# Optimization experiments

Measured on AMD Instinct MI355X. Metric: run time of the kernel, lower is better.

## Reference

```python
import jax, jax.numpy as jnp
import numpy as np

B, T, R = 32, 200, 8192
TOPK_RATIO = 0.05
K = int(R * TOPK_RATIO)            # 409 selected regions
K2 = int(R * TOPK_RATIO ** 2)      # 20 compressed features
REST = R - K                        # 7783 == rest_limitation
BN_EPS = 1e-5
NORM_EPS = 1e-12


def _linear_params(key, fan_in, fan_out):
    kw, kb = jax.random.split(key)
    bound = 1.0 / np.sqrt(fan_in)
    w = jax.random.uniform(kw, (fan_out, fan_in), jnp.float32, -bound, bound)
    b = jax.random.uniform(kb, (fan_out,), jnp.float32, -bound, bound)
    return w, b


def setup_inputs() -> dict:
    key = jax.random.key(0)
    ks = jax.random.split(key, 8)
    x = jax.random.normal(ks[0], (B, T, R), jnp.float32)
    w_proj, b_proj = _linear_params(ks[1], T, 1)
    w_process, b_process = _linear_params(ks[2], K, K)
    w_compress, b_compress = _linear_params(ks[3], K, K2)
    w_unzip, b_unzip = _linear_params(ks[4], K2, K)
    w_unprocess, b_unprocess = _linear_params(ks[5], K, K)
    w_rest, b_rest = _linear_params(ks[6], K, REST)
    bn_gamma = jnp.ones((T,), jnp.float32)
    bn_beta = jnp.zeros((T,), jnp.float32)
    return {
        "x": x,
        "w_proj": w_proj[0], "b_proj": b_proj,
        "w_process": w_process, "b_process": b_process,
        "bn_gamma": bn_gamma, "bn_beta": bn_beta,
        "w_compress": w_compress, "b_compress": b_compress,
        "w_unzip": w_unzip, "b_unzip": b_unzip,
        "w_unprocess": w_unprocess, "b_unprocess": b_unprocess,
        "w_rest": w_rest, "b_rest": b_rest,
    }


def reference(x, w_proj, b_proj, w_process, b_process, bn_gamma, bn_beta,
              w_compress, b_compress, w_unzip, b_unzip,
              w_unprocess, b_unprocess, w_rest, b_rest):
    # ---------------- Encoder ----------------
    border_mask = jnp.isnan(x)                       # [B,T,R]
    x = jnp.where(border_mask, 0.0, x)
    # F.normalize over the time axis (dim=1)
    nrm = jnp.sqrt(jnp.sum(x * x, axis=1, keepdims=True))
    x = x / jnp.maximum(nrm, NORM_EPS)
    # projection: Linear(T,1) on x.transpose(-1,-2) -> score [B,R]
    score = jnp.einsum('btr,t->br', x, w_proj) + b_proj
    border_limit = jnp.mean(border_mask.astype(x.dtype), axis=1)   # [B,R]
    score = jnp.where(border_limit.astype(bool), -10000.0, score)
    _, index = jax.lax.top_k(score, K)               # [B,K] (descending score order)
    x_topk = jnp.take_along_axis(x, index[:, None, :], axis=2)  # [B,T,K]
    sel = jnp.zeros((B, R), x.dtype).at[jnp.arange(B)[:, None], index].set(1.0)
    mask = jnp.broadcast_to(sel[:, None, :], (B, T, R))
    # process: Linear(K,K) + BatchNorm1d(T) in training mode (batch stats)
    h = jnp.einsum('btk,jk->btj', x_topk, w_process) + b_process
    mu = jnp.mean(h, axis=(0, 2), keepdims=True)
    var = jnp.var(h, axis=(0, 2), keepdims=True)     # biased, as torch BN
    h = (h - mu) / jnp.sqrt(var + BN_EPS)
    h = h * bn_gamma[None, :, None] + bn_beta[None, :, None]
    x_compress = jnp.einsum('btk,jk->btj', h, w_compress) + b_compress  # [B,T,K2]

    # ---------------- Decoder ----------------
    z = jnp.einsum('btc,kc->btk', x_compress, w_unzip) + b_unzip
    z = jnp.einsum('btk,jk->btj', z, w_unprocess) + b_unprocess          # [B,T,K]
    z_rest = jnp.einsum('btk,rk->btr', z, w_rest) + b_rest               # [B,T,REST]
    # rest positions: columns neither NaN-bordered nor topk-selected, ascending
    occupied = jnp.logical_or(sel.astype(bool), jnp.any(border_mask, axis=1))  # [B,R]
    rest_pos = jax.vmap(lambda s: jnp.argsort(s)[:REST])(occupied)       # [B,REST]

    def scat(zv, zr, idx, rp):
        xr = jnp.zeros((T, R), zv.dtype)
        xr = xr.at[:, idx].set(zv)
        xr = xr.at[:, rp].set(zr)
        return xr

    x_recon = jax.vmap(scat)(z, z_rest, index, rest_pos)                 # [B,T,R]
    return (x_recon, x_compress, mask, border_mask, index)
```

## Files before the change

### kernel.cpp

```cpp
#include <hip/hip_runtime.h>

#define Bz 32
#define Tz 200
#define Rz 8192
#define Kz 409
#define KP 416
#define K2 20
#define K2P 32
#define RESTz 7783

typedef __bf16 bf16x8 __attribute__((ext_vector_type(8)));
typedef float f32x4 __attribute__((ext_vector_type(4)));

__launch_bounds__(256)
__global__ void k_padcast(const float* __restrict__ src, __bf16* __restrict__ dst,
                          int N, int Kd, int Npad, int Kpad) {
    int i = blockIdx.x * 256 + threadIdx.x;
    int total = Npad * Kpad;
    if (i >= total) return;
    int r = i / Kpad, c = i - r * Kpad;
    float v = (r < N && c < Kd) ? src[(size_t)r * Kd + c] : 0.f;
    dst[i] = (__bf16)v;
}

__launch_bounds__(256)
__global__ void k_wu(const float* __restrict__ wup, const float* __restrict__ wz,
                     const float* __restrict__ b_uz, const float* __restrict__ b_up,
                     float* __restrict__ WU_f, float* __restrict__ bU,
                     __bf16* __restrict__ WU_b) {
    __shared__ float lw[Kz * K2];
    __shared__ float lb[Kz];
    const int tid = threadIdx.x;
    for (int i = tid; i < Kz * K2; i += 256) lw[i] = wz[i];
    for (int i = tid; i < Kz; i += 256) lb[i] = b_uz[i];
    __syncthreads();
    const int r = blockIdx.x * 8 + (tid >> 5);
    const int c = tid & 31;
    if (r >= 512) return;
    if (r >= Kz) {
        WU_b[(size_t)r * K2P + c] = (__bf16)0.f;
        if (c == K2) bU[r] = 0.f;
        return;
    }
    const float* row = wup + (size_t)r * Kz;
    if (c < K2) {
        float a0 = 0.f, a1 = 0.f, a2 = 0.f, a3 = 0.f;
#pragma unroll 4
        for (int j = 0; j < 408; j += 4) {
            a0 = fmaf(row[j],     lw[(j)     * K2 + c], a0);
            a1 = fmaf(row[j + 1], lw[(j + 1) * K2 + c], a1);
            a2 = fmaf(row[j + 2], lw[(j + 2) * K2 + c], a2);
            a3 = fmaf(row[j + 3], lw[(j + 3) * K2 + c], a3);
        }
        a0 = fmaf(row[408], lw[408 * K2 + c], a0);
        float acc = (a0 + a1) + (a2 + a3);
        WU_f[(size_t)r * K2 + c] = acc;
        WU_b[(size_t)r * K2P + c] = (__bf16)acc;
    } else {
        WU_b[(size_t)r * K2P + c] = (__bf16)0.f;
        if (c == K2) {
            float a0 = 0.f, a1 = 0.f, a2 = 0.f, a3 = 0.f;
#pragma unroll 4
            for (int j = 0; j < 408; j += 4) {
                a0 = fmaf(row[j], lb[j], a0);
                a1 = fmaf(row[j + 1], lb[j + 1], a1);
                a2 = fmaf(row[j + 2], lb[j + 2], a2);
                a3 = fmaf(row[j + 3], lb[j + 3], a3);
            }
            a0 = fmaf(row[408], lb[408], a0);
            bU[r] = (a0 + a1) + (a2 + a3) + b_up[r];
        }
    }
}

__launch_bounds__(256)
__global__ void k_wr(const float* __restrict__ wr, const float* __restrict__ b_r,
                     const float* __restrict__ WU_f, const float* __restrict__ bU,
                     __bf16* __restrict__ WR_b, float* __restrict__ bR) {
    __shared__ float lw[Kz * K2];
    __shared__ float lb[Kz];
    const int tid = threadIdx.x;
    for (int i = tid; i < Kz * K2; i += 256) lw[i] = WU_f[i];
    for (int i = tid; i < Kz; i += 256) lb[i] = bU[i];
    __syncthreads();
    const int r = blockIdx.x * 8 + (tid >> 5);
    const int c = tid & 31;
    if (r >= 7808) return;
    if (r >= RESTz) {
        WR_b[(size_t)r * K2P + c] = (__bf16)0.f;
        if (c == K2) bR[r] = 0.f;
        return;
    }
    const float* row = wr + (size_t)r * Kz;
    if (c < K2) {
        float a0 = 0.f, a1 = 0.f, a2 = 0.f, a3 = 0.f;
#pragma unroll 4
        for (int j = 0; j < 408; j += 4) {
            a0 = fmaf(row[j],     lw[(j)     * K2 + c], a0);
            a1 = fmaf(row[j + 1], lw[(j + 1) * K2 + c], a1);
            a2 = fmaf(row[j + 2], lw[(j + 2) * K2 + c], a2);
            a3 = fmaf(row[j + 3], lw[(j + 3) * K2 + c], a3);
        }
        a0 = fmaf(row[408], lw[408 * K2 + c], a0);
        WR_b[(size_t)r * K2P + c] = (__bf16)((a0 + a1) + (a2 + a3));
    } else {
        WR_b[(size_t)r * K2P + c] = (__bf16)0.f;
        if (c == K2) {
            float a0 = 0.f, a1 = 0.f, a2 = 0.f, a3 = 0.f;
#pragma unroll 4
            for (int j = 0; j < 408; j += 4) {
                a0 = fmaf(row[j], lb[j], a0);
                a1 = fmaf(row[j + 1], lb[j + 1], a1);
                a2 = fmaf(row[j + 2], lb[j + 2], a2);
                a3 = fmaf(row[j + 3], lb[j + 3], a3);
            }
            a0 = fmaf(row[408], lb[408], a0);
            bR[r] = (a0 + a1) + (a2 + a3) + b_r[r];
        }
    }
}

__launch_bounds__(256)
__global__ void k_stats(const float* __restrict__ x, const float* __restrict__ w_proj,
                        const float* __restrict__ b_proj,
                        float* __restrict__ invnrm, float* __restrict__ score,
                        int* __restrict__ bordany, float* __restrict__ border_out) {
    const int b = blockIdx.y;
    const int c = blockIdx.x * 256 + threadIdx.x;
    const float* xp = x + (size_t)b * Tz * Rz + c;
    float* bp = border_out + (size_t)b * Tz * Rz + c;
    float p[32];
#pragma unroll
    for (int y = 0; y < 32; ++y) p[y] = 0.f;
    int nn = 0;
    for (int k = 0; k < 7; ++k) {
        const int tbase = k * 32;
#pragma unroll
        for (int y = 0; y < 32; ++y) {
            const int t = tbase + y;
            if (t < Tz) {
                float v = xp[(size_t)t * Rz];
                bool isn = (v != v);
                nn |= isn ? 1 : 0;
                float val = isn ? 0.f : v;
                bp[(size_t)t * Rz] = isn ? 1.0f : 0.0f;
                p[y] = __fadd_rn(p[y], __fmul_rn(val, val));
            }
        }
    }
#pragma unroll
    for (int off = 16; off > 0; off >>= 1)
#pragma unroll
        for (int y = 0; y < 16; ++y)
            if (y < off) p[y] = __fadd_rn(p[y], p[y + off]);
    const float ss = p[0];
    const float nv = fmaxf(__fsqrt_rn(ss), 1e-12f);
    float q[32];
#pragma unroll
    for (int y = 0; y < 32; ++y) q[y] = 0.f;
    for (int k = 0; k < 7; ++k) {
        const int tbase = k * 32;
#pragma unroll
        for (int y = 0; y < 32; ++y) {
            const int t = tbase + y;
            if (t < Tz) {
                float v = xp[(size_t)t * Rz];
                float val = (v != v) ? 0.f : v;
                float xn = __fdiv_rn(val, nv);
                float e = __fmul_rn(xn, w_proj[t]);
                q[y] = __fadd_rn(q[y], e);
            }
        }
    }
#pragma unroll
    for (int off = 16; off > 0; off >>= 1)
#pragma unroll
        for (int y = 0; y < 16; ++y)
            if (y < off) q[y] = __fadd_rn(q[y], q[y + off]);
    float sc = __fadd_rn(q[0], b_proj[0]);
    if (nn) sc = -10000.f;
    invnrm[(size_t)b * Rz + c] = __fdiv_rn(1.0f, nv);
    score[(size_t)b * Rz + c] = sc;
    bordany[(size_t)b * Rz + c] = nn;
}

__launch_bounds__(1024)
__global__ void k_topk(const float* __restrict__ score, const int* __restrict__ bordany,
                       int* __restrict__ index_ws, int* __restrict__ rest_pos,
                       float* __restrict__ o_index) {
    const int b = blockIdx.x;
    const int tid = threadIdx.x;
    __shared__ unsigned su[Rz];
    __shared__ unsigned hist[256];
    __shared__ unsigned sfx[256];
    __shared__ unsigned ckey[512];
    __shared__ unsigned cidx[512];
    __shared__ unsigned cnum;
    __shared__ unsigned sh_prefix;
    __shared__ int sh_need;
    __shared__ int scnt[1024];

    for (int i = tid; i < Rz; i += 1024) {
        unsigned u = __float_as_uint(score[(size_t)b * Rz + i]);
        u = (u & 0x80000000u) ? ~u : (u | 0x80000000u);
        su[i] = u;
    }
    __syncthreads();

    unsigned prefix = 0u, pmask = 0u;
    int need = Kz;
    for (int byte = 3; byte >= 0; --byte) {
        const int sh = byte * 8;
        if (tid < 256) hist[tid] = 0u;
        __syncthreads();
        for (int i = tid; i < Rz; i += 1024) {
            unsigned u = su[i];
            if ((u & pmask) == prefix) atomicAdd(&hist[(u >> sh) & 255u], 1u);
        }
        __syncthreads();
        if (tid < 256) sfx[tid] = hist[tid];
        __syncthreads();
        for (int off = 1; off < 256; off <<= 1) {
            unsigned add = 0u;
            if (tid < 256 && tid + off < 256) add = sfx[tid + off];
            __syncthreads();
            if (tid < 256) sfx[tid] += add;
            __syncthreads();
        }
        if (tid < 256) {
            unsigned above = (tid == 255) ? 0u : sfx[tid + 1];
            if (sfx[tid] >= (unsigned)need && above < (unsigned)need) {
                sh_need = need - (int)above;
                sh_prefix = prefix | ((unsigned)tid << sh);
            }
        }
        __syncthreads();
        prefix = sh_prefix;
        need = sh_need;
        pmask |= (0xFFu << sh);
        __syncthreads();
    }
    const unsigned Tval = prefix;

    if (tid == 0) cnum = 0u;
    __syncthreads();
    for (int i = tid; i < Rz; i += 1024) {
        unsigned u = su[i];
        if (u >= Tval) {
            unsigned p = atomicAdd(&cnum, 1u);
            if (p < 512u) { ckey[p] = u; cidx[p] = (unsigned)i; }
        }
    }
    __syncthreads();
    const int cn = (cnum < 512u) ? (int)cnum : 512;
    for (int i = tid; i < 512; i += 1024)
        if (i >= cn) { ckey[i] = 0u; cidx[i] = 0xFFFFFFFFu; }
    __syncthreads();

    for (int kk = 2; kk <= 512; kk <<= 1) {
        for (int j = kk >> 1; j > 0; j >>= 1) {
            if (tid < 256) {
                const int i = ((tid & ~(j - 1)) << 1) | (tid & (j - 1));
                const int l = i | j;
                unsigned ka = ckey[i], kb = ckey[l];
                unsigned ia = cidx[i], ib = cidx[l];
                bool a_after_b = (ka < kb) || (ka == kb && ia > ib);
                bool b_after_a = (kb < ka) || (kb == ka && ib > ia);
                bool desc = ((i & kk) == 0);
                bool dosw = desc ? a_after_b : b_after_a;
                if (dosw) { ckey[i] = kb; ckey[l] = ka; cidx[i] = ib; cidx[l] = ia; }
            }
            __syncthreads();
        }
    }

    for (int i = tid; i < Kz; i += 1024) {
        int idx = (int)(cidx[i] & 8191u);
        index_ws[b * Kz + i] = idx;
        o_index[(size_t)b * Kz + i] = (float)idx;
    }
    __syncthreads();
    for (int i = tid; i < Rz; i += 1024)
        su[i] = (bordany[(size_t)b * Rz + i] != 0) ? 1u : 0u;
    __syncthreads();
    for (int i = tid; i < Kz; i += 1024) su[cidx[i] & 8191u] = 1u;
    __syncthreads();
    int cnt = 0;
    {
        const int base = tid * 8;
#pragma unroll
        for (int o = 0; o < 8; ++o) cnt += (su[base + o] == 0u) ? 1 : 0;
    }
    scnt[tid] = cnt;
    __syncthreads();
    for (int offp = 1; offp < 1024; offp <<= 1) {
        int add = (tid >= offp) ? scnt[tid - offp] : 0;
        __syncthreads();
        scnt[tid] += add;
        __syncthreads();
    }
    const int total_un = scnt[1023];
    int run = scnt[tid] - cnt;
    const int base = tid * 8;
    for (int o = 0; o < 8; ++o) {
        const int c = base + o;
        const bool un = (su[c] == 0u);
        int pos = un ? run : (total_un + (c - run));
        if (un) run++;
        if (pos < RESTz) rest_pos[b * RESTz + pos] = c;
    }
}

__launch_bounds__(256)
__global__ void k_gather(const float* __restrict__ x, const float* __restrict__ invnrm,
                         const int* __restrict__ index_ws, __bf16* __restrict__ x_topk) {
    const int m = blockIdx.x;
    const int b = m / Tz;
    const float* xrow = x + (size_t)m * Rz;
    for (int kk = threadIdx.x; kk < KP; kk += 256) {
        float val = 0.f;
        if (kk < Kz) {
            const unsigned idx = (unsigned)index_ws[b * Kz + kk] & 8191u;
            float v = xrow[idx];
            if (v != v) v = 0.f;
            val = __fmul_rn(v, invnrm[(size_t)b * Rz + idx]);
        }
        x_topk[(size_t)m * KP + kk] = (__bf16)val;
    }
}

__launch_bounds__(256)
__global__ void k_bn(const __bf16* __restrict__ h, const float* __restrict__ gamma,
                     const float* __restrict__ beta, __bf16* __restrict__ hbn) {
    const int t = blockIdx.x;
    const int tid = threadIdx.x;
    float s = 0.f, s2 = 0.f;
    for (int i = tid; i < Bz * Kz; i += 256) {
        int b = i / Kz, j = i - b * Kz;
        float v = (float)h[(size_t)(b * Tz + t) * KP + j];
        s += v;
        s2 += v * v;
    }
    for (int off = 32; off > 0; off >>= 1) {
        s += __shfl_down(s, off);
        s2 += __shfl_down(s2, off);
    }
    __shared__ float rs[4], rs2[4];
    __shared__ float sc_sh, sf_sh;
    const int wid = tid >> 6;
    if ((tid & 63) == 0) { rs[wid] = s; rs2[wid] = s2; }
    __syncthreads();
    if (tid == 0) {
        float S = rs[0] + rs[1] + rs[2] + rs[3];
        float S2 = rs2[0] + rs2[1] + rs2[2] + rs2[3];
        const float invN = 1.f / (float)(Bz * Kz);
        float mu = S * invN;
        float var = S2 * invN - mu * mu;
        float rstd = rsqrtf(var + 1e-5f);
        float scl = gamma[t] * rstd;
        sc_sh = scl;
        sf_sh = beta[t] - mu * scl;
    }
    __syncthreads();
    const float scl = sc_sh, sft = sf_sh;
    for (int i = tid; i < Bz * KP; i += 256) {
        int b = i / KP, j = i - b * KP;
        float outv = 0.f;
        if (j < Kz) {
            float v = (float)h[(size_t)(b * Tz + t) * KP + j];
            outv = v * scl + sft;
        }
        hbn[(size_t)(b * Tz + t) * KP + j] = (__bf16)outv;
    }
}

__launch_bounds__(256)
__global__ void k_mask(const int* __restrict__ index_ws, float* __restrict__ o_mask) {
    const int bt = blockIdx.x;
    const int b = bt / Tz;
    const int tid = threadIdx.x;
    __shared__ unsigned bm[256];
    bm[tid] = 0u;
    __syncthreads();
    for (int i = tid; i < Kz; i += 256) {
        unsigned idx = (unsigned)index_ws[b * Kz + i] & 8191u;
        atomicOr(&bm[idx >> 5], 1u << (idx & 31u));
    }
    __syncthreads();
    const unsigned bits = bm[tid];
    float* dst = o_mask + (size_t)bt * Rz + tid * 32;
#pragma unroll
    for (int g = 0; g < 8; ++g) {
        float4 v;
        v.x = ((bits >> (g * 4 + 0)) & 1u) ? 1.0f : 0.0f;
        v.y = ((bits >> (g * 4 + 1)) & 1u) ? 1.0f : 0.0f;
        v.z = ((bits >> (g * 4 + 2)) & 1u) ? 1.0f : 0.0f;
        v.w = ((bits >> (g * 4 + 3)) & 1u) ? 1.0f : 0.0f;
        *(float4*)(dst + g * 4) = v;
    }
}

template <int EPI>
__launch_bounds__(256)
__global__ void k_gemm(const __bf16* __restrict__ A, int lda, int ksteps,
                       const __bf16* __restrict__ Wb, int ldb,
                       const float* __restrict__ bias,
                       __bf16* __restrict__ b_out,
                       float* __restrict__ o_xc,
                       const int* __restrict__ index_ws,
                       const int* __restrict__ rest_pos,
                       float* __restrict__ o_recon) {
    __shared__ __bf16 As[128][32];
    __shared__ __bf16 Bs[128][32];
    const int m0 = blockIdx.x * 128;
    const int n0 = blockIdx.y * 128;
    const int tid = threadIdx.x;
    const int lane = tid & 63;
    const int wid = tid >> 6;
    const int wm = wid >> 1, wn = wid & 1;
    const int r0 = lane >> 2;
    const int sg = (lane & 3) * 8;
    const int fr = lane & 15;
    const int fg = lane >> 4;
    f32x4 acc[4][4];
#pragma unroll
    for (int i = 0; i < 4; ++i)
#pragma unroll
        for (int j = 0; j < 4; ++j) {
            f32x4 z = {0.f, 0.f, 0.f, 0.f};
            acc[i][j] = z;
        }

    const int ca = wid * 16 + r0;
    const int cb = (wid + 4) * 16 + r0;
    const __bf16* gA0 = A + (size_t)(m0 + ca) * lda + sg;
    const __bf16* gA1 = A + (size_t)(m0 + cb) * lda + sg;
    const __bf16* gB0 = Wb + (size_t)(n0 + ca) * ldb + sg;
    const __bf16* gB1 = Wb + (size_t)(n0 + cb) * ldb + sg;
    __bf16* lA0 = &As[wid * 16][0];
    __bf16* lA1 = &As[(wid + 4) * 16][0];
    __bf16* lB0 = &Bs[wid * 16][0];
    __bf16* lB1 = &Bs[(wid + 4) * 16][0];

    for (int s = 0; s < ksteps; ++s) {
        const int k0 = s * 32;
        __syncthreads();
        __builtin_amdgcn_global_load_lds(gA0 + k0, lA0, 16, 0, 0);
        __builtin_amdgcn_global_load_lds(gA1 + k0, lA1, 16, 0, 0);
        __builtin_amdgcn_global_load_lds(gB0 + k0, lB0, 16, 0, 0);
        __builtin_amdgcn_global_load_lds(gB1 + k0, lB1, 16, 0, 0);
        __syncthreads();
        bf16x8 af[4], bf[4];
#pragma unroll
        for (int mi = 0; mi < 4; ++mi)
            af[mi] = *(const bf16x8*)&As[wm * 64 + mi * 16 + fr][fg * 8];
#pragma unroll
        for (int ni = 0; ni < 4; ++ni)
            bf[ni] = *(const bf16x8*)&Bs[wn * 64 + ni * 16 + fr][fg * 8];
#pragma unroll
        for (int mi = 0; mi < 4; ++mi)
#pragma unroll
            for (int ni = 0; ni < 4; ++ni)
                acc[mi][ni] = __builtin_amdgcn_mfma_f32_16x16x32_bf16(af[mi], bf[ni],
                                                                      acc[mi][ni], 0, 0, 0);
    }

#pragma unroll
    for (int mi = 0; mi < 4; ++mi)
#pragma unroll
        for (int ni = 0; ni < 4; ++ni)
#pragma unroll
            for (int rr = 0; rr < 4; ++rr) {
                const int gm = m0 + wm * 64 + mi * 16 + fg * 4 + rr;
                const int gn = n0 + wn * 64 + ni * 16 + fr;
                const float v = acc[mi][ni][rr];
                if constexpr (EPI == 0) {
                    if (gn < KP) {
                        float val = (gn < Kz) ? (v + bias[gn]) : 0.f;
                        b_out[(size_t)gm * KP + gn] = (__bf16)val;
                    }
                } else if constexpr (EPI == 1) {
                    if (gn < K2P) {
                        float val = (gn < K2) ? (v + bias[gn]) : 0.f;
                        if (gn < K2) o_xc[(size_t)gm * K2 + gn] = val;
                        b_out[(size_t)gm * K2P + gn] = (__bf16)val;
                    }
                } else if constexpr (EPI == 3) {
                    if (gn < Kz) {
                        float val = v + bias[gn];
                        const int bb = gm / Tz;
                        const unsigned col = (unsigned)index_ws[bb * Kz + gn] & 8191u;
                        o_recon[(size_t)gm * Rz + col] = val;
                    }
                } else {
                    if (gn < RESTz) {
                        const float val = v + bias[gn];
                        const int bb = gm / Tz;
                        const unsigned col = (unsigned)rest_pos[bb * RESTz + gn] & 8191u;
                        o_recon[(size_t)gm * Rz + col] = val;
                    }
                }
            }
}

extern "C" void kernel_launch(void* const* d_in, const int* in_sizes, int n_in,
                              void* d_out, int out_size, void* d_ws, size_t ws_size,
                              hipStream_t stream) {
    (void)in_sizes; (void)n_in; (void)out_size;
    const float* x           = (const float*)d_in[0];
    const float* w_proj      = (const float*)d_in[1];
    const float* b_proj      = (const float*)d_in[2];
    const float* w_process   = (const float*)d_in[3];
    const float* b_process   = (const float*)d_in[4];
    const float* bn_gamma    = (const float*)d_in[5];
    const float* bn_beta     = (const float*)d_in[6];
    const float* w_compress  = (const float*)d_in[7];
    const float* b_compress  = (const float*)d_in[8];
    const float* w_unzip     = (const float*)d_in[9];
    const float* b_unzip     = (const float*)d_in[10];
    const float* w_unprocess = (const float*)d_in[11];
    const float* b_unprocess = (const float*)d_in[12];
    const float* w_rest      = (const float*)d_in[13];
    const float* b_rest      = (const float*)d_in[14];

    float* out = (float*)d_out;
    float* o_recon  = out;
    float* o_xc     = o_recon + (size_t)Bz * Tz * Rz;
    float* o_mask   = o_xc + (size_t)Bz * Tz * K2;
    float* o_border = o_mask + (size_t)Bz * Tz * Rz;
    float* o_index  = o_border + (size_t)Bz * Tz * Rz;

    const size_t SLOT = ((size_t)Bz * Tz * KP * 2 + 255) & ~(size_t)255;
    const size_t IDXB = ((size_t)Bz * Kz * 4 + 255) & ~(size_t)255;
    const size_t RESB = ((size_t)Bz * RESTz * 4 + 255) & ~(size_t)255;
    const size_t WPB  = ((size_t)512 * KP * 2 + 255) & ~(size_t)255;
    const size_t WCB  = ((size_t)128 * KP * 2 + 255) & ~(size_t)255;
    const size_t WUF  = ((size_t)Kz * K2 * 4 + 255) & ~(size_t)255;
    const size_t BUB  = ((size_t)512 * 4 + 255) & ~(size_t)255;
    const size_t WUB  = ((size_t)512 * K2P * 2 + 255) & ~(size_t)255;
    const size_t WRB  = ((size_t)7808 * K2P * 2 + 255) & ~(size_t)255;
    const size_t BRB  = ((size_t)7808 * 4 + 255) & ~(size_t)255;
    const size_t need = 3 * SLOT + IDXB + RESB + WPB + WCB + WUF + BUB + WUB + WRB + BRB;
    if (ws_size < need) return;

    char* ws = (char*)d_ws;
    size_t off = 0;
    auto AL = [&](size_t n) { void* p = ws + off; off += n; return p; };
    __bf16* S1 = (__bf16*)AL(SLOT);
    __bf16* S2 = (__bf16*)AL(SLOT);
    __bf16* S3 = (__bf16*)AL(SLOT);
    int* index_ws = (int*)AL(IDXB);
    int* rest_pos = (int*)AL(RESB);
    __bf16* wp_b  = (__bf16*)AL(WPB);
    __bf16* wc_b  = (__bf16*)AL(WCB);
    float*  WU_f  = (float*)AL(WUF);
    float*  bU    = (float*)AL(BUB);
    __bf16* WU_b  = (__bf16*)AL(WUB);
    __bf16* WR_b  = (__bf16*)AL(WRB);
    float*  bR    = (float*)AL(BRB);

    float* invnrm = (float*)S2;
    float* score  = invnrm + (size_t)Bz * Rz;
    int*   bordany = (int*)(score + (size_t)Bz * Rz);

    __bf16* x_topk = S1;
    __bf16* hbuf   = S2;
    __bf16* hbn    = S3;
    __bf16* xc_pad = S2;
    __bf16* zb     = S1;

    auto PC = [&](const float* src, __bf16* dst, int N, int Kd, int Npad, int Kpad) {
        int total = Npad * Kpad;
        k_padcast<<<dim3((total + 255) / 256), dim3(256), 0, stream>>>(src, dst, N, Kd, Npad, Kpad);
    };
    PC(w_process, wp_b, Kz, Kz, 512, KP);
    PC(w_compress, wc_b, K2, Kz, 128, KP);
    k_wu<<<dim3(64), dim3(256), 0, stream>>>(w_unprocess, w_unzip, b_unzip, b_unprocess,
                                             WU_f, bU, WU_b);
    k_wr<<<dim3(976), dim3(256), 0, stream>>>(w_rest, b_rest, WU_f, bU, WR_b, bR);

    k_stats<<<dim3(Rz / 256, Bz), dim3(256), 0, stream>>>(x, w_proj, b_proj, invnrm, score,
                                                          bordany, o_border);
    k_topk<<<dim3(Bz), dim3(1024), 0, stream>>>(score, bordany, index_ws, rest_pos, o_index);
    k_gather<<<dim3(Bz * Tz), dim3(256), 0, stream>>>(x, invnrm, index_ws, x_topk);

    dim3 blk(256);
    k_gemm<0><<<dim3(50, 4), blk, 0, stream>>>(x_topk, KP, 13, wp_b, KP, b_process,
                                               hbuf, nullptr, nullptr, nullptr, nullptr);
    k_bn<<<dim3(Tz), blk, 0, stream>>>(hbuf, bn_gamma, bn_beta, hbn);
    k_gemm<1><<<dim3(50, 1), blk, 0, stream>>>(hbn, KP, 13, wc_b, KP, b_compress,
                                               xc_pad, o_xc, nullptr, nullptr, nullptr);
    k_gemm<3><<<dim3(50, 4), blk, 0, stream>>>(xc_pad, K2P, 1, WU_b, K2P, bU,
                                               zb, nullptr, index_ws, nullptr, o_recon);
    k_gemm<4><<<dim3(50, 61), blk, 0, stream>>>(xc_pad, K2P, 1, WR_b, K2P, bR,
                                                nullptr, nullptr, nullptr, rest_pos, o_recon);
    k_mask<<<dim3(Bz * Tz), dim3(256), 0, stream>>>(index_ws, o_mask);
}
```

Before: 591.3 us.

## Rework top-k kernel with wave shuffles, rank sort, and 256-thread blocks

Rewrites the per-batch top-k kernel to run on 256 threads instead of 1024. The histogram suffix scan and the free-slot prefix scan now use wave-level shuffles instead of many barrier-separated shared-memory steps. The bitonic sort of candidates is replaced by a counting rank sort in which each candidate scans all the others. This removes most __syncthreads calls, but the rank sort does O(n^2) shared-memory reads and each thread now scans 32 elements serially. The unused zb pointer passed to the decoder GEMM is also dropped.

```diff
diff --git a/kernel.cpp b/kernel.cpp
--- a/kernel.cpp
+++ b/kernel.cpp
@@ -184,53 +184,65 @@
     bordany[(size_t)b * Rz + c] = nn;
 }
 
-__launch_bounds__(1024)
+__launch_bounds__(256)
 __global__ void k_topk(const float* __restrict__ score, const int* __restrict__ bordany,
                        int* __restrict__ index_ws, int* __restrict__ rest_pos,
                        float* __restrict__ o_index) {
     const int b = blockIdx.x;
     const int tid = threadIdx.x;
+    const int lane = tid & 63;
+    const int wv = tid >> 6;
     __shared__ unsigned su[Rz];
     __shared__ unsigned hist[256];
-    __shared__ unsigned sfx[256];
+    __shared__ unsigned sfx[257];
     __shared__ unsigned ckey[512];
     __shared__ unsigned cidx[512];
+    __shared__ unsigned short rnk[512];
     __shared__ unsigned cnum;
     __shared__ unsigned sh_prefix;
     __shared__ int sh_need;
-    __shared__ int scnt[1024];
-
-    for (int i = tid; i < Rz; i += 1024) {
+    __shared__ int wsum[4];
+
+    for (int i = tid; i < Rz; i += 256) {
         unsigned u = __float_as_uint(score[(size_t)b * Rz + i]);
         u = (u & 0x80000000u) ? ~u : (u | 0x80000000u);
         su[i] = u;
     }
+    if (tid == 0) { cnum = 0u; sfx[256] = 0u; }
     __syncthreads();
 
     unsigned prefix = 0u, pmask = 0u;
     int need = Kz;
     for (int byte = 3; byte >= 0; --byte) {
         const int sh = byte * 8;
-        if (tid < 256) hist[tid] = 0u;
-        __syncthreads();
-        for (int i = tid; i < Rz; i += 1024) {
+        hist[tid] = 0u;
+        __syncthreads();
+        for (int i = tid; i < Rz; i += 256) {
             unsigned u = su[i];
             if ((u & pmask) == prefix) atomicAdd(&hist[(u >> sh) & 255u], 1u);
         }
         __syncthreads();
-        if (tid < 256) sfx[tid] = hist[tid];
-        __syncthreads();
-        for (int off = 1; off < 256; off <<= 1) {
-            unsigned add = 0u;
-            if (tid < 256 && tid + off < 256) add = sfx[tid + off];
-            __syncthreads();
-            if (tid < 256) sfx[tid] += add;
-            __syncthreads();
-        }
-        if (tid < 256) {
-            unsigned above = (tid == 255) ? 0u : sfx[tid + 1];
-            if (sfx[tid] >= (unsigned)need && above < (unsigned)need) {
-                sh_need = need - (int)above;
+        if (tid < 64) {
+            unsigned h0 = hist[4 * tid], h1 = hist[4 * tid + 1];
+            unsigned h2 = hist[4 * tid + 2], h3 = hist[4 * tid + 3];
+            unsigned t3 = h3, t2 = h2 + t3, t1 = h1 + t2, t0 = h0 + t1;
+            unsigned U = t0;
+#pragma unroll
+            for (int off = 1; off < 64; off <<= 1) {
+                unsigned u2 = __shfl_down(U, off);
+                if (tid + off < 64) U += u2;
+            }
+            const unsigned T = U - t0;
+            sfx[4 * tid]     = t0 + T;
+            sfx[4 * tid + 1] = t1 + T;
+            sfx[4 * tid + 2] = t2 + T;
+            sfx[4 * tid + 3] = t3 + T;
+        }
+        __syncthreads();
+        {
+            unsigned cur = sfx[tid], nxt = sfx[tid + 1];
+            if (cur >= (unsigned)need && nxt < (unsigned)need) {
+                sh_need = need - (int)nxt;
                 sh_prefix = prefix | ((unsigned)tid << sh);
             }
         }
@@ -242,9 +254,7 @@
     }
     const unsigned Tval = prefix;
 
-    if (tid == 0) cnum = 0u;
-    __syncthreads();
-    for (int i = tid; i < Rz; i += 1024) {
+    for (int i = tid; i < Rz; i += 256) {
         unsigned u = su[i];
         if (u >= Tval) {
             unsigned p = atomicAdd(&cnum, 1u);
@@ -253,56 +263,45 @@
     }
     __syncthreads();
     const int cn = (cnum < 512u) ? (int)cnum : 512;
-    for (int i = tid; i < 512; i += 1024)
-        if (i >= cn) { ckey[i] = 0u; cidx[i] = 0xFFFFFFFFu; }
-    __syncthreads();
-
-    for (int kk = 2; kk <= 512; kk <<= 1) {
-        for (int j = kk >> 1; j > 0; j >>= 1) {
-            if (tid < 256) {
-                const int i = ((tid & ~(j - 1)) << 1) | (tid & (j - 1));
-                const int l = i | j;
-                unsigned ka = ckey[i], kb = ckey[l];
-                unsigned ia = cidx[i], ib = cidx[l];
-                bool a_after_b = (ka < kb) || (ka == kb && ia > ib);
-                bool b_after_a = (kb < ka) || (kb == ka && ib > ia);
-                bool desc = ((i & kk) == 0);
-                bool dosw = desc ? a_after_b : b_after_a;
-                if (dosw) { ckey[i] = kb; ckey[l] = ka; cidx[i] = ib; cidx[l] = ia; }
-            }
-            __syncthreads();
-        }
-    }
-
-    for (int i = tid; i < Kz; i += 1024) {
-        int idx = (int)(cidx[i] & 8191u);
-        index_ws[b * Kz + i] = idx;
-        o_index[(size_t)b * Kz + i] = (float)idx;
-    }
-    __syncthreads();
-    for (int i = tid; i < Rz; i += 1024)
+
+    for (int i = tid; i < cn; i += 256) {
+        const unsigned ki = ckey[i], ii = cidx[i];
+        int r = 0;
+        for (int j = 0; j < cn; ++j) {
+            const unsigned kj = ckey[j];
+            r += (kj > ki || (kj == ki && cidx[j] < ii)) ? 1 : 0;
+        }
+        rnk[i] = (unsigned short)r;
+        if (r < Kz) {
+            index_ws[b * Kz + r] = (int)ii;
+            o_index[(size_t)b * Kz + r] = (float)ii;
+        }
+    }
+    __syncthreads();
+    for (int i = tid; i < Rz; i += 256)
         su[i] = (bordany[(size_t)b * Rz + i] != 0) ? 1u : 0u;
     __syncthreads();
-    for (int i = tid; i < Kz; i += 1024) su[cidx[i] & 8191u] = 1u;
+    for (int i = tid; i < cn; i += 256)
+        if (rnk[i] < Kz) su[cidx[i] & 8191u] = 1u;
     __syncthreads();
     int cnt = 0;
-    {
-        const int base = tid * 8;
-#pragma unroll
-        for (int o = 0; o < 8; ++o) cnt += (su[base + o] == 0u) ? 1 : 0;
-    }
-    scnt[tid] = cnt;
-    __syncthreads();
-    for (int offp = 1; offp < 1024; offp <<= 1) {
-        int add = (tid >= offp) ? scnt[tid - offp] : 0;
-        __syncthreads();
-        scnt[tid] += add;
-        __syncthreads();
-    }
-    const int total_un = scnt[1023];
-    int run = scnt[tid] - cnt;
-    const int base = tid * 8;
-    for (int o = 0; o < 8; ++o) {
+    const int base = tid * 32;
+#pragma unroll
+    for (int o = 0; o < 32; ++o) cnt += (su[base + o] == 0u) ? 1 : 0;
+    int inc = cnt;
+#pragma unroll
+    for (int off = 1; off < 64; off <<= 1) {
+        int v2 = __shfl_up(inc, off);
+        if (lane >= off) inc += v2;
+    }
+    if (lane == 63) wsum[wv] = inc;
+    __syncthreads();
+    int woff = 0;
+    for (int w = 0; w < 4; ++w)
+        if (w < wv) woff += wsum[w];
+    const int total_un = wsum[0] + wsum[1] + wsum[2] + wsum[3];
+    int run = woff + inc - cnt;
+    for (int o = 0; o < 32; ++o) {
         const int c = base + o;
         const bool un = (su[c] == 0u);
         int pos = un ? run : (total_un + (c - run));
@@ -567,7 +566,6 @@
     __bf16* hbuf   = S2;
     __bf16* hbn    = S3;
     __bf16* xc_pad = S2;
-    __bf16* zb     = S1;
 
     auto PC = [&](const float* src, __bf16* dst, int N, int Kd, int Npad, int Kpad) {
         int total = Npad * Kpad;
@@ -581,7 +579,7 @@
 
     k_stats<<<dim3(Rz / 256, Bz), dim3(256), 0, stream>>>(x, w_proj, b_proj, invnrm, score,
                                                           bordany, o_border);
-    k_topk<<<dim3(Bz), dim3(1024), 0, stream>>>(score, bordany, index_ws, rest_pos, o_index);
+    k_topk<<<dim3(Bz), dim3(256), 0, stream>>>(score, bordany, index_ws, rest_pos, o_index);
     k_gather<<<dim3(Bz * Tz), dim3(256), 0, stream>>>(x, invnrm, index_ws, x_topk);
 
     dim3 blk(256);
@@ -591,7 +589,7 @@
     k_gemm<1><<<dim3(50, 1), blk, 0, stream>>>(hbn, KP, 13, wc_b, KP, b_compress,
                                                xc_pad, o_xc, nullptr, nullptr, nullptr);
     k_gemm<3><<<dim3(50, 4), blk, 0, stream>>>(xc_pad, K2P, 1, WU_b, K2P, bU,
-                                               zb, nullptr, index_ws, nullptr, o_recon);
+                                               nullptr, nullptr, index_ws, nullptr, o_recon);
     k_gemm<4><<<dim3(50, 61), blk, 0, stream>>>(xc_pad, K2P, 1, WR_b, K2P, bR,
                                                 nullptr, nullptr, nullptr, rest_pos, o_recon);
     k_mask<<<dim3(Bz * Tz), dim3(256), 0, stream>>>(index_ws, o_mask);
```

Result: slower. 610.0 us (+3.2%).

## Fuse decoder GEMMs, scatter and mask into one column-indexed recon kernel

Applied to the files above, without the earlier changes.

Top-k now emits a per-column source map (rest position, selected index, or zero) plus a mask flag, in place of the rest_pos list. A single new kernel gathers the right weight row for each output column, runs a small MFMA over K2P, and writes o_recon and o_mask with coalesced stores. This replaces two scatter-writing GEMMs and a separate mask kernel. The goal is to drop scattered uncoalesced writes to the large output and one full pass. In exchange, weight rows are gathered per column block, and columns with no source (NaN-bordered) get explicit zeros written.

```diff
diff --git a/kernel.cpp b/kernel.cpp
--- a/kernel.cpp
+++ b/kernel.cpp
@@ -186,7 +186,7 @@
 
 __launch_bounds__(1024)
 __global__ void k_topk(const float* __restrict__ score, const int* __restrict__ bordany,
-                       int* __restrict__ index_ws, int* __restrict__ rest_pos,
+                       int* __restrict__ index_ws, int* __restrict__ colsrc,
                        float* __restrict__ o_index) {
     const int b = blockIdx.x;
     const int tid = threadIdx.x;
@@ -283,7 +283,7 @@
     for (int i = tid; i < Rz; i += 1024)
         su[i] = (bordany[(size_t)b * Rz + i] != 0) ? 1u : 0u;
     __syncthreads();
-    for (int i = tid; i < Kz; i += 1024) su[cidx[i] & 8191u] = 1u;
+    for (int i = tid; i < Kz; i += 1024) su[cidx[i] & 8191u] = 2u + (unsigned)i;
     __syncthreads();
     int cnt = 0;
     {
@@ -304,10 +304,16 @@
     const int base = tid * 8;
     for (int o = 0; o < 8; ++o) {
         const int c = base + o;
-        const bool un = (su[c] == 0u);
+        const unsigned s = su[c];
+        const bool un = (s == 0u);
         int pos = un ? run : (total_un + (c - run));
         if (un) run++;
-        if (pos < RESTz) rest_pos[b * RESTz + pos] = c;
+        int src;
+        if (pos < RESTz) src = 0x20000000 | pos;
+        else if (s >= 2u) src = 0x10000000 | (int)(s - 2u);
+        else src = 0;
+        if (s >= 2u) src |= 0x40000000;
+        colsrc[b * Rz + c] = src;
     }
 }
 
@@ -375,29 +381,79 @@
 }
 
 __launch_bounds__(256)
-__global__ void k_mask(const int* __restrict__ index_ws, float* __restrict__ o_mask) {
-    const int bt = blockIdx.x;
-    const int b = bt / Tz;
+__global__ void k_recon(const __bf16* __restrict__ xc, const __bf16* __restrict__ WU_b,
+                        const __bf16* __restrict__ WR_b, const float* __restrict__ bU,
+                        const float* __restrict__ bR, const int* __restrict__ colsrc,
+                        float* __restrict__ o_recon, float* __restrict__ o_mask) {
+    __shared__ __bf16 As[64][32];
+    __shared__ __bf16 Bs[128][32];
+    __shared__ float biasv[128];
+    __shared__ float maskv[128];
+    const int n0 = blockIdx.x * 128;
+    const int m0 = blockIdx.y * 64;
+    const int b = blockIdx.z;
     const int tid = threadIdx.x;
-    __shared__ unsigned bm[256];
-    bm[tid] = 0u;
-    __syncthreads();
-    for (int i = tid; i < Kz; i += 256) {
-        unsigned idx = (unsigned)index_ws[b * Kz + i] & 8191u;
-        atomicOr(&bm[idx >> 5], 1u << (idx & 31u));
-    }
-    __syncthreads();
-    const unsigned bits = bm[tid];
-    float* dst = o_mask + (size_t)bt * Rz + tid * 32;
-#pragma unroll
-    for (int g = 0; g < 8; ++g) {
-        float4 v;
-        v.x = ((bits >> (g * 4 + 0)) & 1u) ? 1.0f : 0.0f;
-        v.y = ((bits >> (g * 4 + 1)) & 1u) ? 1.0f : 0.0f;
-        v.z = ((bits >> (g * 4 + 2)) & 1u) ? 1.0f : 0.0f;
-        v.w = ((bits >> (g * 4 + 3)) & 1u) ? 1.0f : 0.0f;
-        *(float4*)(dst + g * 4) = v;
-    }
+    const int lane = tid & 63;
+    const int w = tid >> 6;
+    {
+        const int row = tid >> 2, seg = (tid & 3) * 8;
+        const int t = m0 + row;
+        bf16x8 v = {};
+        if (t < Tz) v = *(const bf16x8*)(xc + ((size_t)b * Tz + t) * K2P + seg);
+        *(bf16x8*)&As[row][seg] = v;
+    }
+    {
+        const int col = tid >> 1, half = tid & 1;
+        const int s = colsrc[b * Rz + n0 + col];
+        const __bf16* srcrow = nullptr;
+        float bv = 0.f;
+        if (s & 0x20000000) {
+            const int p = s & 0xFFFF;
+            srcrow = WR_b + (size_t)p * K2P;
+            bv = bR[p];
+        } else if (s & 0x10000000) {
+            const int k = s & 0xFFFF;
+            srcrow = WU_b + (size_t)k * K2P;
+            bv = bU[k];
+        }
+        bf16x8 v0 = {}, v1 = {};
+        if (srcrow) {
+            v0 = *(const bf16x8*)(srcrow + half * 16);
+            v1 = *(const bf16x8*)(srcrow + half * 16 + 8);
+        }
+        *(bf16x8*)&Bs[col][half * 16] = v0;
+        *(bf16x8*)&Bs[col][half * 16 + 8] = v1;
+        if (half == 0) {
+            biasv[col] = bv;
+            maskv[col] = (s & 0x40000000) ? 1.0f : 0.0f;
+        }
+    }
+    __syncthreads();
+    const int fr = lane & 15, fg = lane >> 4;
+    bf16x8 af = *(const bf16x8*)&As[w * 16 + fr][fg * 8];
+    f32x4 acc[8];
+#pragma unroll
+    for (int ni = 0; ni < 8; ++ni) {
+        f32x4 z = {0.f, 0.f, 0.f, 0.f};
+        acc[ni] = z;
+    }
+#pragma unroll
+    for (int ni = 0; ni < 8; ++ni) {
+        bf16x8 bf = *(const bf16x8*)&Bs[ni * 16 + fr][fg * 8];
+        acc[ni] = __builtin_amdgcn_mfma_f32_16x16x32_bf16(af, bf, acc[ni], 0, 0, 0);
+    }
+#pragma unroll
+    for (int ni = 0; ni < 8; ++ni)
+#pragma unroll
+        for (int rr = 0; rr < 4; ++rr) {
+            const int t = m0 + w * 16 + fg * 4 + rr;
+            if (t < Tz) {
+                const int cl = ni * 16 + fr;
+                const size_t o = ((size_t)(b * Tz + t)) * Rz + n0 + cl;
+                o_recon[o] = acc[ni][rr] + biasv[cl];
+                o_mask[o] = maskv[cl];
+            }
+        }
 }
 
 template <int EPI>
@@ -406,10 +462,7 @@
                        const __bf16* __restrict__ Wb, int ldb,
                        const float* __restrict__ bias,
                        __bf16* __restrict__ b_out,
-                       float* __restrict__ o_xc,
-                       const int* __restrict__ index_ws,
-                       const int* __restrict__ rest_pos,
-                       float* __restrict__ o_recon) {
+                       float* __restrict__ o_xc) {
     __shared__ __bf16 As[128][32];
     __shared__ __bf16 Bs[128][32];
     const int m0 = blockIdx.x * 128;
@@ -479,25 +532,11 @@
                         float val = (gn < Kz) ? (v + bias[gn]) : 0.f;
                         b_out[(size_t)gm * KP + gn] = (__bf16)val;
                     }
-                } else if constexpr (EPI == 1) {
+                } else {
                     if (gn < K2P) {
                         float val = (gn < K2) ? (v + bias[gn]) : 0.f;
                         if (gn < K2) o_xc[(size_t)gm * K2 + gn] = val;
                         b_out[(size_t)gm * K2P + gn] = (__bf16)val;
-                    }
-                } else if constexpr (EPI == 3) {
-                    if (gn < Kz) {
-                        float val = v + bias[gn];
-                        const int bb = gm / Tz;
-                        const unsigned col = (unsigned)index_ws[bb * Kz + gn] & 8191u;
-                        o_recon[(size_t)gm * Rz + col] = val;
-                    }
-                } else {
-                    if (gn < RESTz) {
-                        const float val = v + bias[gn];
-                        const int bb = gm / Tz;
-                        const unsigned col = (unsigned)rest_pos[bb * RESTz + gn] & 8191u;
-                        o_recon[(size_t)gm * Rz + col] = val;
                     }
                 }
             }
@@ -532,7 +571,7 @@
 
     const size_t SLOT = ((size_t)Bz * Tz * KP * 2 + 255) & ~(size_t)255;
     const size_t IDXB = ((size_t)Bz * Kz * 4 + 255) & ~(size_t)255;
-    const size_t RESB = ((size_t)Bz * RESTz * 4 + 255) & ~(size_t)255;
+    const size_t CSB  = ((size_t)Bz * Rz * 4 + 255) & ~(size_t)255;
     const size_t WPB  = ((size_t)512 * KP * 2 + 255) & ~(size_t)255;
     const size_t WCB  = ((size_t)128 * KP * 2 + 255) & ~(size_t)255;
     const size_t WUF  = ((size_t)Kz * K2 * 4 + 255) & ~(size_t)255;
@@ -540,7 +579,7 @@
     const size_t WUB  = ((size_t)512 * K2P * 2 + 255) & ~(size_t)255;
     const size_t WRB  = ((size_t)7808 * K2P * 2 + 255) & ~(size_t)255;
     const size_t BRB  = ((size_t)7808 * 4 + 255) & ~(size_t)255;
-    const size_t need = 3 * SLOT + IDXB + RESB + WPB + WCB + WUF + BUB + WUB + WRB + BRB;
+    const size_t need = 3 * SLOT + IDXB + CSB + WPB + WCB + WUF + BUB + WUB + WRB + BRB;
     if (ws_size < need) return;
 
     char* ws = (char*)d_ws;
@@ -550,7 +589,7 @@
     __bf16* S2 = (__bf16*)AL(SLOT);
     __bf16* S3 = (__bf16*)AL(SLOT);
     int* index_ws = (int*)AL(IDXB);
-    int* rest_pos = (int*)AL(RESB);
+    int* colsrc   = (int*)AL(CSB);
     __bf16* wp_b  = (__bf16*)AL(WPB);
     __bf16* wc_b  = (__bf16*)AL(WCB);
     float*  WU_f  = (float*)AL(WUF);
@@ -567,7 +606,6 @@
     __bf16* hbuf   = S2;
     __bf16* hbn    = S3;
     __bf16* xc_pad = S2;
-    __bf16* zb     = S1;
 
     auto PC = [&](const float* src, __bf16* dst, int N, int Kd, int Npad, int Kpad) {
         int total = Npad * Kpad;
@@ -581,18 +619,15 @@
 
     k_stats<<<dim3(Rz / 256, Bz), dim3(256), 0, stream>>>(x, w_proj, b_proj, invnrm, score,
                                                           bordany, o_border);
-    k_topk<<<dim3(Bz), dim3(1024), 0, stream>>>(score, bordany, index_ws, rest_pos, o_index);
+    k_topk<<<dim3(Bz), dim3(1024), 0, stream>>>(score, bordany, index_ws, colsrc, o_index);
     k_gather<<<dim3(Bz * Tz), dim3(256), 0, stream>>>(x, invnrm, index_ws, x_topk);
 
     dim3 blk(256);
     k_gemm<0><<<dim3(50, 4), blk, 0, stream>>>(x_topk, KP, 13, wp_b, KP, b_process,
-                                               hbuf, nullptr, nullptr, nullptr, nullptr);
+                                               hbuf, nullptr);
     k_bn<<<dim3(Tz), blk, 0, stream>>>(hbuf, bn_gamma, bn_beta, hbn);
     k_gemm<1><<<dim3(50, 1), blk, 0, stream>>>(hbn, KP, 13, wc_b, KP, b_compress,
-                                               xc_pad, o_xc, nullptr, nullptr, nullptr);
-    k_gemm<3><<<dim3(50, 4), blk, 0, stream>>>(xc_pad, K2P, 1, WU_b, K2P, bU,
-                                               zb, nullptr, index_ws, nullptr, o_recon);
-    k_gemm<4><<<dim3(50, 61), blk, 0, stream>>>(xc_pad, K2P, 1, WR_b, K2P, bR,
-                                                nullptr, nullptr, nullptr, rest_pos, o_recon);
-    k_mask<<<dim3(Bz * Tz), dim3(256), 0, stream>>>(index_ws, o_mask);
-}
+                                               xc_pad, o_xc);
+    k_recon<<<dim3(64, 4, Bz), blk, 0, stream>>>(xc_pad, WU_b, WR_b, bU, bR, colsrc,
+                                                 o_recon, o_mask);
+}
```

After: 494.1 us. -16.4%, faster.
